# Performance work log

Hardware: AMD Instinct MI355X
Metric: run time of the kernel (lower is better)

## Reference

```python
import jax, jax.numpy as jnp
import numpy as np

H = 16      # how_many_heads
DH = 64     # dimension_of_head
D_K = 1024  # dimension_of_key (input dim); scaler = sqrt(D_K), faithful to source
NEG = -np.finfo(np.float32).max


def setup_inputs() -> dict:
    key0 = jax.random.key(0)
    ks = jax.random.split(key0, 8)
    B, S, D = 2, 2048, 1024
    query = jax.random.normal(ks[0], (B, S, D), dtype=jnp.float32)
    key_in = jax.random.normal(ks[1], (B, S, D), dtype=jnp.float32)
    value = jax.random.normal(ks[2], (B, S, D), dtype=jnp.float32)
    mask = jax.random.bernoulli(ks[3], 0.5, (B, S, S))  # bool, True = masked
    # nn.Linear(in, out, bias=False): y = x @ W^T with W:[out,in]; store [in,out] directly
    sc = 1.0 / np.sqrt(D)
    W_q = jax.random.normal(ks[4], (D, H * DH), dtype=jnp.float32) * sc
    W_k = jax.random.normal(ks[5], (D, H * DH), dtype=jnp.float32) * sc
    W_v = jax.random.normal(ks[6], (D, H * DH), dtype=jnp.float32) * sc
    W_o = jax.random.normal(ks[7], (H * DH, D), dtype=jnp.float32) * sc
    return {"query": query, "key": key_in, "value": value, "mask": mask,
            "W_q": W_q, "W_k": W_k, "W_v": W_v, "W_o": W_o}


def reference(query, key, value, mask, W_q, W_k, W_v, W_o):
    B, Sq, _ = query.shape
    # project and split heads: [B, S, H, DH] -> [B, H, S, DH]
    q = (query @ W_q).reshape(B, Sq, H, DH).transpose(0, 2, 1, 3)
    k = (key @ W_k).reshape(B, -1, H, DH).transpose(0, 2, 1, 3)
    v = (value @ W_v).reshape(B, -1, H, DH).transpose(0, 2, 1, 3)
    # scores: [B, H, Sq, Sk], scaled by sqrt(dimension_of_key)=sqrt(D_K)
    scores = jnp.einsum('bhqd,bhkd->bhqk', q, k) / np.float32(np.sqrt(D_K))
    # mask: [B, Sq, Sk] -> [B, H, Sq, Sk]; masked_fill with -finfo(float32).max
    scores = jnp.where(mask[:, None, :, :], NEG, scores)
    # FAITHFUL to source: softmax over dim=2 (the QUERY axis of the 4D tensor)
    attn = jax.nn.softmax(scores, axis=2)
    hidden = jnp.einsum('bhqk,bhkd->bhqd', attn, v)  # [B, H, Sq, DH]
    hidden = hidden.transpose(0, 2, 1, 3).reshape(B, Sq, H * DH) @ W_o
    return hidden, k, v
```

## Files before the change

kernel.cpp:

```cpp
#include <hip/hip_runtime.h>
#include <hip/hip_bf16.h>

#define BB 2
#define SS 2048
#define DD 1024
#define HH 16
#define DHH 64

#define SCLOG2E 0.045084221f

typedef unsigned short u16;
typedef unsigned int   u32;
typedef __bf16 bf16_t;
typedef bf16_t bf16x8 __attribute__((ext_vector_type(8)));
typedef u16    u16x8  __attribute__((ext_vector_type(8)));
typedef u32    u32x4v __attribute__((ext_vector_type(4)));
typedef float  f32x4  __attribute__((ext_vector_type(4)));

#define MFMA(a,b,c) __builtin_amdgcn_mfma_f32_16x16x32_bf16(a,b,c,0,0,0)

#define SW(c,r)  ((c) ^ ((r) & 7))
#define SW3(c,r) ((c) ^ ((r) & 3))

typedef __attribute__((address_space(1))) const unsigned int as1_u32;
typedef __attribute__((address_space(3))) unsigned int as3_u32;

__device__ __forceinline__ void gld16(const void* g, void* l){
  __builtin_amdgcn_global_load_lds((as1_u32*)g, (as3_u32*)l, 16, 0, 0);
}

__device__ __forceinline__ u16 f2bf(float f){
  u32 u = __builtin_bit_cast(u32, f);
  u32 r = (u + 0x7fffu + ((u >> 16) & 1u)) >> 16;
  return (u16)r;
}
__device__ __forceinline__ u16 nbf(float f){
  bf16_t b = (bf16_t)f;
  return __builtin_bit_cast(u16, b);
}
__device__ __forceinline__ float bf2f(u16 v){
  u32 u = ((u32)v) << 16;
  return __builtin_bit_cast(float, u);
}
__device__ __forceinline__ bf16x8 ldb8(const u16* p){
  return __builtin_bit_cast(bf16x8, *(const u16x8*)p);
}

__device__ __forceinline__ void stage64(const u16* __restrict__ g0, int stride,
                                        u16* lds0, int tid){
  int w = tid >> 6, lane = tid & 63;
  #pragma unroll
  for (int j = 0; j < 2; j++){
    int slot = j*256 + w*64 + lane;
    int row = slot >> 3, c = slot & 7;
    gld16(g0 + (size_t)row*stride + (SW(c,row) << 3),
          lds0 + (size_t)(j*256 + w*64)*8);
  }
}

__device__ __forceinline__ void stage32(const u16* __restrict__ g0, int stride,
                                        u16* lds0, int tid){
  int w = tid >> 6, lane = tid & 63;
  #pragma unroll
  for (int j = 0; j < 2; j++){
    int slot = j*256 + w*64 + lane;
    int row = slot >> 2, c = slot & 3;
    gld16(g0 + (size_t)row*stride + (SW3(c,row) << 3),
          lds0 + (size_t)(j*256 + w*64)*8);
  }
}

__global__ __launch_bounds__(256) void cvt3(const float* __restrict__ s0,
                                            const float* __restrict__ s1,
                                            const float* __restrict__ s2,
                                            u16* __restrict__ d0,
                                            u16* __restrict__ d1,
                                            u16* __restrict__ d2){
  const float* s = blockIdx.z == 0 ? s0 : (blockIdx.z == 1 ? s1 : s2);
  u16*         d = blockIdx.z == 0 ? d0 : (blockIdx.z == 1 ? d1 : d2);
  size_t i = ((size_t)blockIdx.x*256 + threadIdx.x) * 8;
  const float4* p = (const float4*)(s + i);
  float4 x = p[0], y = p[1];
  u16x8 u;
  u[0]=f2bf(x.x); u[1]=f2bf(x.y); u[2]=f2bf(x.z); u[3]=f2bf(x.w);
  u[4]=f2bf(y.x); u[5]=f2bf(y.y); u[6]=f2bf(y.z); u[7]=f2bf(y.w);
  *(u16x8*)(d + i) = u;
}

__global__ __launch_bounds__(256) void detect_mask(const u32* mw, u32* flag){
  __shared__ int fBig, fFloat;
  if (threadIdx.x == 0){ fBig = 0; fFloat = 0; }
  __syncthreads();
  for (int i = threadIdx.x; i < 4096; i += 256){
    u32 w = mw[i];
    if (w == 0x3f800000u) fFloat = 1;
    else if (w > 1u) fBig = 1;
  }
  __syncthreads();
  if (threadIdx.x == 0) *flag = fFloat ? 2u : (fBig ? 1u : 0u);
}

__device__ __forceinline__ u32 pack32(const void* mask, u32 f, size_t e0){
  u32 bits = 0;
  if (f == 1u){
    const uchar4* mb = (const uchar4*)((const unsigned char*)mask + e0);
    #pragma unroll
    for (int j = 0; j < 8; j++){
      uchar4 v = mb[j];
      bits |= (v.x?1u:0u) << (4*j)   | (v.y?1u:0u) << (4*j+1)
            | (v.z?1u:0u) << (4*j+2) | (v.w?1u:0u) << (4*j+3);
    }
  } else if (f == 0u){
    const int4* mi = (const int4*)((const int*)mask + e0);
    #pragma unroll
    for (int j = 0; j < 8; j++){
      int4 v = mi[j];
      bits |= (v.x?1u:0u) << (4*j)   | (v.y?1u:0u) << (4*j+1)
            | (v.z?1u:0u) << (4*j+2) | (v.w?1u:0u) << (4*j+3);
    }
  } else {
    const float4* mf = (const float4*)((const float*)mask + e0);
    #pragma unroll
    for (int j = 0; j < 8; j++){
      float4 v = mf[j];
      bits |= (v.x!=0.f?1u:0u) << (4*j)   | (v.y!=0.f?1u:0u) << (4*j+1)
            | (v.z!=0.f?1u:0u) << (4*j+2) | (v.w!=0.f?1u:0u) << (4*j+3);
    }
  }
  return bits;
}

__global__ __launch_bounds__(256) void pack_maskT(const void* __restrict__ mask,
                                                  const u32* __restrict__ flag,
                                                  u32* __restrict__ pmT){
  __shared__ u32 tile[16][65];
  u32 f = *flag;
  int b = blockIdx.y;
  int q0 = blockIdx.x * 16;
  int kw = threadIdx.x & 63, qr = threadIdx.x >> 6;
  #pragma unroll
  for (int i = 0; i < 4; i++){
    int row = i*4 + qr;
    size_t e0 = ((size_t)(b*SS + q0 + row))*SS + kw*32;
    tile[row][kw] = pack32(mask, f, e0);
  }
  __syncthreads();
  int q = threadIdx.x & 15, kw0 = threadIdx.x >> 4;
  #pragma unroll
  for (int i = 0; i < 4; i++){
    int kww = i*16 + kw0;
    pmT[((size_t)b*64 + kww)*SS + q0 + q] = tile[q][kww];
  }
}

__global__ __launch_bounds__(256) void prep_w(const float* __restrict__ W0,
                                              const float* __restrict__ W1,
                                              const float* __restrict__ W2,
                                              const float* __restrict__ W3,
                                              u16* __restrict__ Wt){
  const float* Ws[4] = {W0, W1, W2, W3};
  const float* W = Ws[blockIdx.z];
  float scl = (blockIdx.z == 0) ? SCLOG2E : 1.0f;
  u16* O = Wt + (size_t)blockIdx.z * DD * DD;
  __shared__ float tile[64][65];
  int kb = blockIdx.x * 64, nb = blockIdx.y * 64;
  int col = threadIdx.x & 63, rr = threadIdx.x >> 6;
  #pragma unroll
  for (int i = 0; i < 16; i++){
    int row = i*4 + rr;
    tile[row][col] = W[(size_t)(kb+row)*DD + nb + col];
  }
  __syncthreads();
  #pragma unroll
  for (int i = 0; i < 16; i++){
    int row = i*4 + rr;
    O[(size_t)(nb+row)*DD + kb + col] = f2bf(tile[col][row] * scl);
  }
}

struct GA { const u16* A; const u16* Bt; u16* Cb; float* Co; int mode; };

__global__ __launch_bounds__(256) void gemm32(GA a0, GA a1, GA a2){
  GA ga = blockIdx.z == 0 ? a0 : (blockIdx.z == 1 ? a1 : a2);
  __shared__ u16 As[2][128*32];
  __shared__ u16 Bs[2][128*32];
  int mb = blockIdx.x * 128, nb = blockIdx.y * 128;
  int tid = threadIdx.x, w = tid >> 6, lane = tid & 63, ln = lane & 15, g = lane >> 4;
  int wr = w >> 1, wc = w & 1;
  f32x4 acc[4][4];
  #pragma unroll
  for (int i = 0; i < 4; i++)
    #pragma unroll
    for (int j = 0; j < 4; j++) acc[i][j] = (f32x4){0,0,0,0};

  stage32(ga.A  + (size_t)mb*DD, DD, As[0], tid);
  stage32(ga.Bt + (size_t)nb*DD, DD, Bs[0], tid);
  __syncthreads();
  int buf = 0;
  for (int t = 0; t < 32; t++){
    if (t < 31){
      stage32(ga.A  + (size_t)mb*DD + (t+1)*32, DD, As[buf^1], tid);
      stage32(ga.Bt + (size_t)nb*DD + (t+1)*32, DD, Bs[buf^1], tid);
    }
    bf16x8 av[4], bv[4];
    #pragma unroll
    for (int mf = 0; mf < 4; mf++){
      int row = wr*64 + mf*16 + ln;
      av[mf] = ldb8(&As[buf][row*32 + (SW3(g,row) << 3)]);
    }
    #pragma unroll
    for (int nf = 0; nf < 4; nf++){
      int row = wc*64 + nf*16 + ln;
      bv[nf] = ldb8(&Bs[buf][row*32 + (SW3(g,row) << 3)]);
    }
    #pragma unroll
    for (int mf = 0; mf < 4; mf++)
      #pragma unroll
      for (int nf = 0; nf < 4; nf++)
        acc[mf][nf] = MFMA(av[mf], bv[nf], acc[mf][nf]);
    __syncthreads();
    buf ^= 1;
  }
  #pragma unroll
  for (int mf = 0; mf < 4; mf++){
    #pragma unroll
    for (int nf = 0; nf < 4; nf++){
      #pragma unroll
      for (int r = 0; r < 4; r++){
        int row = mb + wr*64 + mf*16 + g*4 + r;
        int col = nb + wc*64 + nf*16 + ln;
        float v = acc[mf][nf][r];
        if (ga.mode != 2)
          ga.Cb[(size_t)row*DD + col] = f2bf(v);
        if (ga.mode == 1){
          int b_ = row >> 11, s_ = row & (SS-1);
          int h_ = col >> 6,  d_ = col & 63;
          ga.Co[(((size_t)(b_*HH + h_))*SS + s_)*DHH + d_] = v;
        }
        if (ga.mode == 2)
          ga.Co[(size_t)row*DD + col] = v;
      }
    }
  }
}

__global__ __launch_bounds__(256) void pass1_sum(const u16* __restrict__ Qb,
                                                 const u16* __restrict__ Kb,
                                                 const u32* __restrict__ pmT,
                                                 float* __restrict__ cO){
  __shared__ u16 Qst[2][64*64];
  int flat = blockIdx.x + (SS/128)*(blockIdx.y + HH*blockIdx.z);
  int sw = (flat & 7)*64 + (flat >> 3);
  int kblk = (sw & 15) * 128;
  int rest = sw >> 4;
  int h = rest & 15, b = rest >> 4;
  int tid = threadIdx.x, w = tid >> 6, lane = tid & 63, ln = lane & 15, g = lane >> 4;
  bf16x8 kf[2][2];
  #pragma unroll
  for (int f = 0; f < 2; f++){
    const u16* kp = Kb + ((size_t)b*SS + kblk + w*32 + f*16 + ln)*DD + h*DHH + g*8;
    kf[f][0] = ldb8(kp); kf[f][1] = ldb8(kp + 32);
  }
  float cr[2][4] = {{0,0,0,0},{0,0,0,0}};

  stage64(Qb + ((size_t)b*SS)*DD + h*DHH, DD, Qst[0], tid);
  __syncthreads();
  int buf = 0;
  const u32* pmw = pmT + ((size_t)b*64 + (kblk >> 5) + w)*SS;
  for (int t = 0; t < 32; t++){
    if (t < 31) stage64(Qb + ((size_t)b*SS + (t+1)*64)*DD + h*DHH, DD, Qst[buf^1], tid);
    #pragma unroll
    for (int qc = 0; qc < 4; qc++){
      int row = qc*16 + ln;
      bf16x8 b0 = ldb8(&Qst[buf][row*64 + (SW(g,  row) << 3)]);
      bf16x8 b1 = ldb8(&Qst[buf][row*64 + (SW(g+4,row) << 3)]);
      int q = t*64 + qc*16 + ln;
      u32 mw = pmw[q];
      #pragma unroll
      for (int f = 0; f < 2; f++){
        f32x4 sf = {0,0,0,0};
        sf = MFMA(kf[f][0], b0, sf);
        sf = MFMA(kf[f][1], b1, sf);
        #pragma unroll
        for (int r = 0; r < 4; r++){
          float e = __builtin_amdgcn_exp2f(sf[r]);
          cr[f][r] += ((mw >> (f*16 + g*4 + r)) & 1u) ? 0.f : e;
        }
      }
    }
    __syncthreads();
    buf ^= 1;
  }
  #pragma unroll
  for (int f = 0; f < 2; f++)
    #pragma unroll
    for (int r = 0; r < 4; r++){
      #pragma unroll
      for (int msk = 1; msk < 16; msk <<= 1)
        cr[f][r] += __shfl_xor(cr[f][r], msk, 64);
    }
  if (ln == 0){
    #pragma unroll
    for (int f = 0; f < 2; f++)
      #pragma unroll
      for (int r = 0; r < 4; r++)
        cO[((size_t)b*HH + h)*SS + kblk + w*32 + f*16 + g*4 + r] = cr[f][r];
  }
}

__global__ __launch_bounds__(256) void scale_v(const u16* __restrict__ Vb,
                                               const float* __restrict__ cI,
                                               u16* __restrict__ Vt){
  int b = blockIdx.z, h = blockIdx.y;
  int st = blockIdx.x * 64;
  __shared__ u16 tile[64][72];
  int col = threadIdx.x & 63, rr = threadIdx.x >> 6;
  #pragma unroll
  for (int i = 0; i < 16; i++){
    int row = i*4 + rr;
    int s = st + row;
    float inv = 1.0f / cI[((size_t)b*HH + h)*SS + s];
    float v = bf2f(Vb[((size_t)b*SS + s)*DD + h*DHH + col]);
    tile[row][col] = f2bf(v * inv);
  }
  __syncthreads();
  int pc = (col & 32) + ((col >> 2) & 3)*8 + ((col >> 4) & 1)*4 + (col & 3);
  #pragma unroll
  for (int i = 0; i < 16; i++){
    int row = i*4 + rr;
    Vt[(((size_t)b*HH + h)*DHH + row)*SS + st + pc] = tile[col][row];
  }
}

#define P2_QK(PMP, NXT, KP) { \
  u32 _ml[2], _mh[2]; \
  _Pragma("unroll") for (int f = 0; f < 2; f++){ \
    _ml[f] = (PMP)[f*16]; \
    _mh[f] = (PMP)[SS + f*16]; \
  } \
  _Pragma("unroll") for (int kc = 0; kc < 4; kc++){ \
    bf16x8 a0 = ldb8(&KP[koff[kc][0]]); \
    bf16x8 a1 = ldb8(&KP[koff[kc][1]]); \
    _Pragma("unroll") for (int f = 0; f < 2; f++){ \
      f32x4 sf = {0,0,0,0}; \
      sf = MFMA(a0, qf[f][0], sf); \
      sf = MFMA(a1, qf[f][1], sf); \
      u32 mword = (kc < 2) ? _ml[f] : _mh[f]; \
      int msh = (kc & 1) * 16 + g*4; \
      float p0 = ((mword >> (msh+0)) & 1u) ? 0.f : __builtin_amdgcn_exp2f(sf[0]); \
      float p1 = ((mword >> (msh+1)) & 1u) ? 0.f : __builtin_amdgcn_exp2f(sf[1]); \
      float p2 = ((mword >> (msh+2)) & 1u) ? 0.f : __builtin_amdgcn_exp2f(sf[2]); \
      float p3 = ((mword >> (msh+3)) & 1u) ? 0.f : __builtin_amdgcn_exp2f(sf[3]); \
      NXT[f][kc*2]   = (u32)nbf(p0) | ((u32)nbf(p1) << 16); \
      NXT[f][kc*2+1] = (u32)nbf(p2) | ((u32)nbf(p3) << 16); \
    } \
  } }

#define P2_PV(CUR, VP) \
  _Pragma("unroll") for (int kh = 0; kh < 2; kh++){ \
    bf16x8 pa[2]; \
    _Pragma("unroll") for (int f = 0; f < 2; f++) \
      pa[f] = __builtin_bit_cast(bf16x8, \
        (u32x4v){CUR[f][4*kh], CUR[f][4*kh+1], CUR[f][4*kh+2], CUR[f][4*kh+3]}); \
    _Pragma("unroll") for (int df = 0; df < 4; df++){ \
      bf16x8 bv = ldb8(&VP[voff[kh][df]]); \
      _Pragma("unroll") for (int f = 0; f < 2; f++) \
        acc[f][df] = MFMA(pa[f], bv, acc[f][df]); \
    } \
  }

#define P2_BODY(TT, CUR, NXT) \
  __syncthreads(); \
  if ((TT) < 30){ \
    stage64(Kg + (size_t)((TT)+2)*64*DD, DD, K2, tid); \
    stage64(Vth + ((TT)+2)*64,           SS, V2, tid); \
  } \
  if ((TT) < 31) P2_QK(pmq, NXT, K1) \
  P2_PV(CUR, V0) \
  { u16* _tp=K0; K0=K1; K1=K2; K2=_tp; _tp=V0; V0=V1; V1=V2; V2=_tp; pmq += 2*SS; }

__global__ __launch_bounds__(256) void pass2_pv(const u16* __restrict__ Qb,
                                                const u16* __restrict__ Kb,
                                                const u16* __restrict__ Vt,
                                                const u32* __restrict__ pmT,
                                                u16* __restrict__ Hb){
  __shared__ u16 Kst[3][64*64];
  __shared__ u16 Vst[3][64*64];
  int flat = blockIdx.x + (SS/128)*(blockIdx.y + HH*blockIdx.z);
  int sw = (flat & 7)*64 + (flat >> 3);
  int qt = (sw & 15) * 128;
  int rest = sw >> 4;
  int h = rest & 15, b = rest >> 4;
  int tid = threadIdx.x, w = tid >> 6, lane = tid & 63, ln = lane & 15, g = lane >> 4;
  bf16x8 qf[2][2];
  #pragma unroll
  for (int f = 0; f < 2; f++){
    const u16* qp = Qb + ((size_t)b*SS + qt + w*32 + f*16 + ln)*DD + h*DHH + g*8;
    qf[f][0] = ldb8(qp); qf[f][1] = ldb8(qp + 32);
  }
  f32x4 acc[2][4];
  #pragma unroll
  for (int f = 0; f < 2; f++)
    #pragma unroll
    for (int d = 0; d < 4; d++) acc[f][d] = (f32x4){0,0,0,0};

  const u16* Kg  = Kb + ((size_t)b*SS)*DD + h*DHH;
  const u16* Vth = Vt + ((size_t)b*HH + h)*DHH*SS;
  const u32* pmq = pmT + (size_t)b*64*SS + (qt + w*32 + ln);

  int koff[4][2], voff[2][4];
  #pragma unroll
  for (int kc = 0; kc < 4; kc++){
    int row = kc*16 + ln;
    koff[kc][0] = row*64 + (SW(g,  row) << 3);
    koff[kc][1] = row*64 + (SW(g+4,row) << 3);
  }
  #pragma unroll
  for (int kh = 0; kh < 2; kh++)
    #pragma unroll
    for (int df = 0; df < 4; df++){
      int row = df*16 + ln;
      voff[kh][df] = row*64 + (SW(kh*4+g, row) << 3);
    }

  u16 *K0=&Kst[0][0], *K1=&Kst[1][0], *K2=&Kst[2][0];
  u16 *V0=&Vst[0][0], *V1=&Vst[1][0], *V2=&Vst[2][0];
  u32 pkA[2][8], pkB[2][8];

  stage64(Kg,  DD, K0, tid);
  stage64(Vth, SS, V0, tid);
  __syncthreads();
  P2_QK(pmq, pkA, K0)
  pmq += 2*SS;
  stage64(Kg + 64*DD, DD, K1, tid);
  stage64(Vth + 64,   SS, V1, tid);

  #pragma unroll 1
  for (int t = 0; t < 32; t += 2){
    P2_BODY(t,   pkA, pkB)
    P2_BODY(t+1, pkB, pkA)
  }

  #pragma unroll
  for (int f = 0; f < 2; f++)
    #pragma unroll
    for (int df = 0; df < 4; df++)
      #pragma unroll
      for (int r = 0; r < 4; r++){
        int row = qt + w*32 + f*16 + g*4 + r;
        int col = h*DHH + df*16 + ln;
        Hb[((size_t)b*SS + row)*DD + col] = f2bf(acc[f][df][r]);
      }
}

extern "C" void kernel_launch(void* const* d_in, const int* in_sizes, int n_in,
                              void* d_out, int out_size, void* d_ws, size_t ws_size,
                              hipStream_t stream){
  (void)in_sizes; (void)n_in; (void)out_size; (void)ws_size;
  const float* query = (const float*)d_in[0];
  const float* key   = (const float*)d_in[1];
  const float* value = (const float*)d_in[2];
  const void*  mask  = d_in[3];
  const float* W_q = (const float*)d_in[4];
  const float* W_k = (const float*)d_in[5];
  const float* W_v = (const float*)d_in[6];
  const float* W_o = (const float*)d_in[7];

  float* out   = (float*)d_out;
  float* out_h = out;
  float* out_k = out   + (size_t)BB*HH*SS*DHH;
  float* out_v = out_k + (size_t)BB*HH*SS*DHH;

  char* w = (char*)d_ws;
  u16*   Wt  = (u16*)(w);
  u16*   Av  = (u16*)(w + (size_t)( 8u<<20));
  u16*   Qb  = (u16*)(w + (size_t)(16u<<20));
  u16*   Kb  = (u16*)(w + (size_t)(24u<<20));
  u16*   Vb  = (u16*)(w + (size_t)(32u<<20));
  u16*   Vt  = (u16*)(w + (size_t)(40u<<20));
  float* cS  = (float*)(w + (size_t)(48u<<20));
  u32*   pmT = (u32*)(w + (size_t)(48u<<20) + (512u<<10));
  u32*   flag= (u32*)(w + (size_t)(48u<<20) + (1664u<<10));
  u16*   Hb  = Av;
  u16*   Aq  = (u16*)out_h;
  u16*   Ak  = Aq + (size_t)BB*SS*DD;

  detect_mask<<<dim3(1), dim3(256), 0, stream>>>((const u32*)mask, flag);
  pack_maskT<<<dim3(SS/16, BB), dim3(256), 0, stream>>>(mask, flag, pmT);
  prep_w<<<dim3(16,16,4), dim3(256), 0, stream>>>(W_q, W_k, W_v, W_o, Wt);

  cvt3<<<dim3(2048,1,3), dim3(256), 0, stream>>>(query, key, value, Aq, Ak, Av);

  GA gq = { Aq, Wt,             Qb, nullptr, 0 };
  GA gk = { Ak, Wt + 1*1048576, Kb, out_k,   1 };
  GA gv = { Av, Wt + 2*1048576, Vb, out_v,   1 };
  gemm32<<<dim3(32,8,3), dim3(256), 0, stream>>>(gq, gk, gv);

  pass1_sum<<<dim3(SS/128, HH, BB), dim3(256), 0, stream>>>(Qb, Kb, pmT, cS);
  scale_v<<<dim3(SS/64, HH, BB), dim3(256), 0, stream>>>(Vb, cS, Vt);
  pass2_pv<<<dim3(SS/128, HH, BB), dim3(256), 0, stream>>>(Qb, Kb, Vt, pmT, Hb);

  GA go = { Hb, Wt + 3*1048576, nullptr, out_h, 2 };
  gemm32<<<dim3(32,8,1), dim3(256), 0, stream>>>(go, go, go);
}
```

Before: 218.6 us.

## Merge preprocessing kernels and fuse V scaling into the column-sum pass

```diff
diff --git a/kernel.cpp b/kernel.cpp
--- a/kernel.cpp
+++ b/kernel.cpp
@@ -68,23 +68,6 @@
     gld16(g0 + (size_t)row*stride + (SW3(c,row) << 3),
           lds0 + (size_t)(j*256 + w*64)*8);
   }
-}
-
-__global__ __launch_bounds__(256) void cvt3(const float* __restrict__ s0,
-                                            const float* __restrict__ s1,
-                                            const float* __restrict__ s2,
-                                            u16* __restrict__ d0,
-                                            u16* __restrict__ d1,
-                                            u16* __restrict__ d2){
-  const float* s = blockIdx.z == 0 ? s0 : (blockIdx.z == 1 ? s1 : s2);
-  u16*         d = blockIdx.z == 0 ? d0 : (blockIdx.z == 1 ? d1 : d2);
-  size_t i = ((size_t)blockIdx.x*256 + threadIdx.x) * 8;
-  const float4* p = (const float4*)(s + i);
-  float4 x = p[0], y = p[1];
-  u16x8 u;
-  u[0]=f2bf(x.x); u[1]=f2bf(x.y); u[2]=f2bf(x.z); u[3]=f2bf(x.w);
-  u[4]=f2bf(y.x); u[5]=f2bf(y.y); u[6]=f2bf(y.z); u[7]=f2bf(y.w);
-  *(u16x8*)(d + i) = u;
 }
 
 __global__ __launch_bounds__(256) void detect_mask(const u32* mw, u32* flag){
@@ -130,51 +113,68 @@
   return bits;
 }
 
-__global__ __launch_bounds__(256) void pack_maskT(const void* __restrict__ mask,
-                                                  const u32* __restrict__ flag,
-                                                  u32* __restrict__ pmT){
-  __shared__ u32 tile[16][65];
-  u32 f = *flag;
-  int b = blockIdx.y;
-  int q0 = blockIdx.x * 16;
-  int kw = threadIdx.x & 63, qr = threadIdx.x >> 6;
-  #pragma unroll
-  for (int i = 0; i < 4; i++){
-    int row = i*4 + qr;
-    size_t e0 = ((size_t)(b*SS + q0 + row))*SS + kw*32;
-    tile[row][kw] = pack32(mask, f, e0);
-  }
-  __syncthreads();
-  int q = threadIdx.x & 15, kw0 = threadIdx.x >> 4;
-  #pragma unroll
-  for (int i = 0; i < 4; i++){
-    int kww = i*16 + kw0;
-    pmT[((size_t)b*64 + kww)*SS + q0 + q] = tile[q][kww];
-  }
-}
-
-__global__ __launch_bounds__(256) void prep_w(const float* __restrict__ W0,
-                                              const float* __restrict__ W1,
-                                              const float* __restrict__ W2,
-                                              const float* __restrict__ W3,
-                                              u16* __restrict__ Wt){
-  const float* Ws[4] = {W0, W1, W2, W3};
-  const float* W = Ws[blockIdx.z];
-  float scl = (blockIdx.z == 0) ? SCLOG2E : 1.0f;
-  u16* O = Wt + (size_t)blockIdx.z * DD * DD;
-  __shared__ float tile[64][65];
-  int kb = blockIdx.x * 64, nb = blockIdx.y * 64;
-  int col = threadIdx.x & 63, rr = threadIdx.x >> 6;
-  #pragma unroll
-  for (int i = 0; i < 16; i++){
-    int row = i*4 + rr;
-    tile[row][col] = W[(size_t)(kb+row)*DD + nb + col];
-  }
-  __syncthreads();
-  #pragma unroll
-  for (int i = 0; i < 16; i++){
-    int row = i*4 + rr;
-    O[(size_t)(nb+row)*DD + kb + col] = f2bf(tile[col][row] * scl);
+__global__ __launch_bounds__(256) void prep_all(
+    const float* __restrict__ qs, const float* __restrict__ ks,
+    const float* __restrict__ vs,
+    u16* __restrict__ Aq, u16* __restrict__ Ak, u16* __restrict__ Av,
+    const float* __restrict__ W0, const float* __restrict__ W1,
+    const float* __restrict__ W2, const float* __restrict__ W3,
+    u16* __restrict__ Wt,
+    const void* __restrict__ mask, const u32* __restrict__ flag,
+    u32* __restrict__ pmT){
+  __shared__ float shmem[64*65];
+  int bx = blockIdx.x;
+  if (bx < 6144){
+    int zc = bx >> 11, xb = bx & 2047;
+    const float* s = zc == 0 ? qs : (zc == 1 ? ks : vs);
+    u16*         d = zc == 0 ? Aq : (zc == 1 ? Ak : Av);
+    size_t i = ((size_t)xb*256 + threadIdx.x) * 8;
+    const float4* p = (const float4*)(s + i);
+    float4 x = p[0], y = p[1];
+    u16x8 u;
+    u[0]=f2bf(x.x); u[1]=f2bf(x.y); u[2]=f2bf(x.z); u[3]=f2bf(x.w);
+    u[4]=f2bf(y.x); u[5]=f2bf(y.y); u[6]=f2bf(y.z); u[7]=f2bf(y.w);
+    *(u16x8*)(d + i) = u;
+  } else if (bx < 7168){
+    int id = bx - 6144;
+    int z = id >> 8, rem = id & 255;
+    int kb = (rem & 15) * 64, nb = (rem >> 4) * 64;
+    const float* Ws[4] = {W0, W1, W2, W3};
+    const float* W = Ws[z];
+    float scl = (z == 0) ? SCLOG2E : 1.0f;
+    u16* O = Wt + (size_t)z * DD * DD;
+    float (*tile)[65] = (float(*)[65])shmem;
+    int col = threadIdx.x & 63, rr = threadIdx.x >> 6;
+    #pragma unroll
+    for (int i = 0; i < 16; i++){
+      int row = i*4 + rr;
+      tile[row][col] = W[(size_t)(kb+row)*DD + nb + col];
+    }
+    __syncthreads();
+    #pragma unroll
+    for (int i = 0; i < 16; i++){
+      int row = i*4 + rr;
+      O[(size_t)(nb+row)*DD + kb + col] = f2bf(tile[col][row] * scl);
+    }
+  } else {
+    int id = bx - 7168;
+    int q0 = (id & 127) * 16, b = id >> 7;
+    u32 f = *flag;
+    u32 (*tile)[65] = (u32(*)[65])shmem;
+    int kw = threadIdx.x & 63, qr = threadIdx.x >> 6;
+    #pragma unroll
+    for (int i = 0; i < 4; i++){
+      int row = i*4 + qr;
+      size_t e0 = ((size_t)(b*SS + q0 + row))*SS + kw*32;
+      tile[row][kw] = pack32(mask, f, e0);
+    }
+    __syncthreads();
+    int q = threadIdx.x & 15, kw0 = threadIdx.x >> 4;
+    #pragma unroll
+    for (int i = 0; i < 4; i++){
+      int kww = i*16 + kw0;
+      pmT[((size_t)b*64 + kww)*SS + q0 + q] = tile[q][kww];
+    }
   }
 }
 
@@ -244,11 +244,13 @@
   }
 }
 
-__global__ __launch_bounds__(256) void pass1_sum(const u16* __restrict__ Qb,
-                                                 const u16* __restrict__ Kb,
-                                                 const u32* __restrict__ pmT,
-                                                 float* __restrict__ cO){
+__global__ __launch_bounds__(256) void pass1_sv(const u16* __restrict__ Qb,
+                                                const u16* __restrict__ Kb,
+                                                const u32* __restrict__ pmT,
+                                                const u16* __restrict__ Vb,
+                                                u16* __restrict__ Vt){
   __shared__ u16 Qst[2][64*64];
+  __shared__ float cs[128];
   int flat = blockIdx.x + (SS/128)*(blockIdx.y + HH*blockIdx.z);
   int sw = (flat & 7)*64 + (flat >> 3);
   int kblk = (sw & 15) * 128;
@@ -304,31 +306,30 @@
     for (int f = 0; f < 2; f++)
       #pragma unroll
       for (int r = 0; r < 4; r++)
-        cO[((size_t)b*HH + h)*SS + kblk + w*32 + f*16 + g*4 + r] = cr[f][r];
-  }
-}
-
-__global__ __launch_bounds__(256) void scale_v(const u16* __restrict__ Vb,
-                                               const float* __restrict__ cI,
-                                               u16* __restrict__ Vt){
-  int b = blockIdx.z, h = blockIdx.y;
-  int st = blockIdx.x * 64;
-  __shared__ u16 tile[64][72];
-  int col = threadIdx.x & 63, rr = threadIdx.x >> 6;
-  #pragma unroll
-  for (int i = 0; i < 16; i++){
-    int row = i*4 + rr;
-    int s = st + row;
-    float inv = 1.0f / cI[((size_t)b*HH + h)*SS + s];
-    float v = bf2f(Vb[((size_t)b*SS + s)*DD + h*DHH + col]);
-    tile[row][col] = f2bf(v * inv);
+        cs[w*32 + f*16 + g*4 + r] = cr[f][r];
   }
   __syncthreads();
-  int pc = (col & 32) + ((col >> 2) & 3)*8 + ((col >> 4) & 1)*4 + (col & 3);
-  #pragma unroll
-  for (int i = 0; i < 16; i++){
-    int row = i*4 + rr;
-    Vt[(((size_t)b*HH + h)*DHH + row)*SS + st + pc] = tile[col][row];
+
+  u16 (*vt)[72] = (u16(*)[72])&Qst[0][0];
+  int col = tid & 63, rr = tid >> 6;
+  #pragma unroll 1
+  for (int ch = 0; ch < 2; ch++){
+    int st = kblk + ch*64;
+    #pragma unroll
+    for (int i = 0; i < 16; i++){
+      int row = i*4 + rr;
+      float inv = 1.0f / cs[ch*64 + row];
+      float v = bf2f(Vb[((size_t)b*SS + st + row)*DD + h*DHH + col]);
+      vt[row][col] = f2bf(v * inv);
+    }
+    __syncthreads();
+    int pc = (col & 32) + ((col >> 2) & 3)*8 + ((col >> 4) & 1)*4 + (col & 3);
+    #pragma unroll
+    for (int i = 0; i < 16; i++){
+      int row = i*4 + rr;
+      Vt[(((size_t)b*HH + h)*DHH + row)*SS + st + pc] = vt[col][row];
+    }
+    __syncthreads();
   }
 }
 
@@ -478,7 +479,6 @@
   u16*   Kb  = (u16*)(w + (size_t)(24u<<20));
   u16*   Vb  = (u16*)(w + (size_t)(32u<<20));
   u16*   Vt  = (u16*)(w + (size_t)(40u<<20));
-  float* cS  = (float*)(w + (size_t)(48u<<20));
   u32*   pmT = (u32*)(w + (size_t)(48u<<20) + (512u<<10));
   u32*   flag= (u32*)(w + (size_t)(48u<<20) + (1664u<<10));
   u16*   Hb  = Av;
@@ -486,18 +486,16 @@
   u16*   Ak  = Aq + (size_t)BB*SS*DD;
 
   detect_mask<<<dim3(1), dim3(256), 0, stream>>>((const u32*)mask, flag);
-  pack_maskT<<<dim3(SS/16, BB), dim3(256), 0, stream>>>(mask, flag, pmT);
-  prep_w<<<dim3(16,16,4), dim3(256), 0, stream>>>(W_q, W_k, W_v, W_o, Wt);
-
-  cvt3<<<dim3(2048,1,3), dim3(256), 0, stream>>>(query, key, value, Aq, Ak, Av);
+  prep_all<<<dim3(7424), dim3(256), 0, stream>>>(query, key, value, Aq, Ak, Av,
+                                                 W_q, W_k, W_v, W_o, Wt,
+                                                 mask, flag, pmT);
 
   GA gq = { Aq, Wt,             Qb, nullptr, 0 };
   GA gk = { Ak, Wt + 1*1048576, Kb, out_k,   1 };
   GA gv = { Av, Wt + 2*1048576, Vb, out_v,   1 };
   gemm32<<<dim3(32,8,3), dim3(256), 0, stream>>>(gq, gk, gv);
 
-  pass1_sum<<<dim3(SS/128, HH, BB), dim3(256), 0, stream>>>(Qb, Kb, pmT, cS);
-  scale_v<<<dim3(SS/64, HH, BB), dim3(256), 0, stream>>>(Vb, cS, Vt);
+  pass1_sv<<<dim3(SS/128, HH, BB), dim3(256), 0, stream>>>(Qb, Kb, pmT, Vb, Vt);
   pass2_pv<<<dim3(SS/128, HH, BB), dim3(256), 0, stream>>>(Qb, Kb, Vt, pmT, Hb);
 
   GA go = { Hb, Wt + 3*1048576, nullptr, out_h, 2 };
```

Result: no change. 222.9 us (+2.0%).
